# Performance work log

Measured on AMD Instinct MI355X. Metric: run time of the kernel, lower is better.

The kernel has to match this reference:

```python
import jax, jax.numpy as jnp
import numpy as np

SPATIAL_SHAPES = [(160, 160), (80, 80), (40, 40)]
D_MODEL = 256
N_HEADS = 8
N_LEVELS = 3
N_POINTS = 4
B = 1
SEQ = sum(h * w for h, w in SPATIAL_SHAPES)  # 33600


def setup_inputs() -> dict:
    key = jax.random.key(0)
    ks = jax.random.split(key, 10)
    f = jax.random.normal
    return {
        "hidden_states": f(ks[0], (B, SEQ, D_MODEL), jnp.float32),
        "encoder_hidden_states": f(ks[1], (B, SEQ, D_MODEL), jnp.float32),
        "position_embeddings": f(ks[2], (B, SEQ, D_MODEL), jnp.float32),
        "reference_points": jax.random.uniform(ks[3], (B, SEQ, N_LEVELS, 2), jnp.float32),
        "Wv": f(ks[4], (D_MODEL, D_MODEL), jnp.float32) * 0.02,
        "bv": jnp.zeros((D_MODEL,), jnp.float32),
        "Ws": f(ks[5], (N_HEADS * N_LEVELS * N_POINTS * 2, D_MODEL), jnp.float32) * 0.02,
        "bs": f(ks[6], (N_HEADS * N_LEVELS * N_POINTS * 2,), jnp.float32) * 2.0,
        "Wa": f(ks[7], (N_HEADS * N_LEVELS * N_POINTS, D_MODEL), jnp.float32) * 0.02,
        "ba": jnp.zeros((N_HEADS * N_LEVELS * N_POINTS,), jnp.float32),
        "Wo": f(ks[8], (D_MODEL, D_MODEL), jnp.float32) * 0.02,
        "bo": jnp.zeros((D_MODEL,), jnp.float32),
    }


def grid_sample_bilinear(img, grid):
    """torch.nn.functional.grid_sample, mode='bilinear', padding_mode='zeros', align_corners=False.
    img: [N, C, Hi, Wi]; grid: [N, Hg, Wg, 2] with (x, y) in [-1, 1]. Returns [N, C, Hg, Wg]."""
    N, C, Hi, Wi = img.shape
    x = (grid[..., 0] + 1.0) * (Wi * 0.5) - 0.5  # unnormalized pixel coords
    y = (grid[..., 1] + 1.0) * (Hi * 0.5) - 0.5
    x0f = jnp.floor(x)
    y0f = jnp.floor(y)
    x0 = x0f.astype(jnp.int32)
    y0 = y0f.astype(jnp.int32)
    wx1 = x - x0f
    wy1 = y - y0f
    imgc = jnp.transpose(img, (0, 2, 3, 1))  # [N, Hi, Wi, C]
    n_idx = jnp.arange(N)[:, None, None]

    def tap(xi, yi, w):
        valid = (xi >= 0) & (xi < Wi) & (yi >= 0) & (yi < Hi)
        xc = jnp.clip(xi, 0, Wi - 1)
        yc = jnp.clip(yi, 0, Hi - 1)
        v = imgc[n_idx, yc, xc]  # [N, Hg, Wg, C]
        return v * (w * valid.astype(img.dtype))[..., None]

    out = (tap(x0, y0, (1.0 - wx1) * (1.0 - wy1))
           + tap(x0 + 1, y0, wx1 * (1.0 - wy1))
           + tap(x0, y0 + 1, (1.0 - wx1) * wy1)
           + tap(x0 + 1, y0 + 1, wx1 * wy1))
    return jnp.transpose(out, (0, 3, 1, 2))  # [N, C, Hg, Wg]


def reference(hidden_states, encoder_hidden_states, position_embeddings, reference_points,
              Wv, bv, Ws, bs, Wa, ba, Wo, bo):
    hd = D_MODEL // N_HEADS
    LP = N_LEVELS * N_POINTS
    Q = SEQ

    hs = hidden_states + position_embeddings  # [B, Q, D]
    value = (encoder_hidden_states @ Wv.T + bv).reshape(B, SEQ, N_HEADS, hd)
    offsets = (hs @ Ws.T + bs).reshape(B * Q, N_HEADS, LP, 2)
    attn = jax.nn.softmax((hs @ Wa.T + ba).reshape(B, Q, N_HEADS, LP), axis=-1)

    # offset normalizer: [w, h] per level, broadcast over points
    norm = jnp.array([[w, h] for (h, w) in SPATIAL_SHAPES], jnp.float32)  # [L, 2]
    norm = jnp.broadcast_to(norm[:, None, :], (N_LEVELS, N_POINTS, 2)).reshape(1, 1, LP, 2)
    rp = reference_points.reshape(-1, N_LEVELS, 1, 2)
    rp = jnp.broadcast_to(rp, (B * Q, N_LEVELS, N_POINTS, 2)).reshape(B * Q, 1, LP, 2)
    loc = rp + offsets / norm                # [BQ, H, LP, 2]
    grids = 2.0 * loc - 1.0

    attn_t = jnp.transpose(attn, (0, 2, 1, 3)).reshape(B * N_HEADS, 1, Q, LP)

    sampled = []
    start = 0
    for lvl, (h, w) in enumerate(SPATIAL_SHAPES):
        v = value[:, start:start + h * w].reshape(B, h * w, N_HEADS * hd)
        v = jnp.transpose(v, (0, 2, 1)).reshape(B * N_HEADS, hd, h, w)
        g = jnp.transpose(grids[:, :, lvl * N_POINTS:(lvl + 1) * N_POINTS], (1, 0, 2, 3))  # [H, BQ, P, 2] (B=1)
        sampled.append(grid_sample_bilinear(v, g))  # [B*H, hd, Q, P]
        start += h * w

    out = (jnp.concatenate(sampled, axis=-1) * attn_t).sum(-1)  # [B*H, hd, Q]
    out = jnp.transpose(out.reshape(B, N_HEADS * hd, Q), (0, 2, 1))  # [B, Q, D]
    output = out @ Wo.T + bo
    return output, attn
```

## Files before the change

kernel.cpp:

```cpp
#include <hip/hip_runtime.h>
#include <math.h>

#define QSEQ 33600
#define NHEADS 8

typedef __attribute__((ext_vector_type(8))) short short8;
typedef __attribute__((ext_vector_type(4))) float floatx4;
typedef unsigned short ushort_t;

static __device__ __forceinline__ ushort_t f2bf(float f) {
  unsigned u = __float_as_uint(f);
  return (ushort_t)((u + 0x7FFF + ((u >> 16) & 1)) >> 16);
}

static __device__ __forceinline__ void gload_lds16(const void* g, void* l) {
  __builtin_amdgcn_global_load_lds((__attribute__((address_space(1))) void*)g,
                                   (__attribute__((address_space(3))) void*)l, 16, 0, 0);
}

template <int MODE>
__global__ __launch_bounds__(256) void gemm_mfma2(
    const ushort_t* __restrict__ A, const ushort_t* __restrict__ Wb,
    const float* __restrict__ bias, void* __restrict__ Cp, int N) {
  __shared__ ushort_t smem[12288];
  ushort_t* As = smem;
  ushort_t* Bs = smem + 4096;

  const int tid = threadIdx.x;
  const int m0 = blockIdx.y * 64;
  const int n0 = blockIdx.x * 128;
  const int wv = tid >> 6, lane = tid & 63;
  const int wm = wv >> 1, wn = wv & 1;
  const int l16 = lane & 15, quad = lane >> 4;

  const int ca0 = wv * 128 + lane, ca1 = ca0 + 64;
  const int ar0 = ca0 >> 3, ar1 = ca1 >> 3;
  const int ak0 = ((ca0 & 7) ^ (ar0 & 7)) * 8;
  const int ak1 = ((ca1 & 7) ^ (ar1 & 7)) * 8;
  const ushort_t* gA0 = A + (size_t)(m0 + ar0) * 256 + ak0;
  const ushort_t* gA1 = A + (size_t)(m0 + ar1) * 256 + ak1;
  ushort_t* lA0 = As + (wv * 128) * 8;
  ushort_t* lA1 = As + (wv * 128 + 64) * 8;

  const ushort_t* gB[4];
  ushort_t* lB[4];
#pragma unroll
  for (int j = 0; j < 4; ++j) {
    const int cb = wv * 256 + j * 64 + lane;
    const int br = cb >> 3;
    const int bk = ((cb & 7) ^ (br & 7)) * 8;
    gB[j] = Wb + (size_t)(n0 + br) * 256 + bk;
    lB[j] = Bs + (wv * 256 + j * 64) * 8;
  }

  floatx4 acc[2][4];
#pragma unroll
  for (int i = 0; i < 2; ++i)
#pragma unroll
    for (int j = 0; j < 4; ++j) acc[i][j] = (floatx4)(0.f);

  const int ra0 = wm * 32 + l16, ra1 = ra0 + 16;
  const int rb0 = wn * 64 + l16;
  const int l8 = l16 & 7;

  for (int k0 = 0; k0 < 256; k0 += 64) {
    gload_lds16(gA0 + k0, lA0);
    gload_lds16(gA1 + k0, lA1);
#pragma unroll
    for (int j = 0; j < 4; ++j) gload_lds16(gB[j] + k0, lB[j]);
    __syncthreads();
#pragma unroll
    for (int k32 = 0; k32 < 2; ++k32) {
      const int cx = ((k32 * 4 + quad) ^ l8) * 8;
      short8 a[2], b[4];
      a[0] = *(const short8*)&As[ra0 * 64 + cx];
      a[1] = *(const short8*)&As[ra1 * 64 + cx];
#pragma unroll
      for (int j = 0; j < 4; ++j)
        b[j] = *(const short8*)&Bs[(rb0 + j * 16) * 64 + cx];
#pragma unroll
      for (int mi = 0; mi < 2; ++mi)
#pragma unroll
        for (int ni = 0; ni < 4; ++ni)
          acc[mi][ni] = __builtin_amdgcn_mfma_f32_16x16x32_bf16(a[mi], b[ni], acc[mi][ni], 0, 0, 0);
    }
    __syncthreads();
  }

  if (MODE == 0) {
    float* C = (float*)Cp;
#pragma unroll
    for (int ni = 0; ni < 4; ++ni) {
      const int col = n0 + wn * 64 + ni * 16 + l16;
      if (col < N) {
        const float bia = bias[col];
#pragma unroll
        for (int mi = 0; mi < 2; ++mi) {
          const int rr = m0 + wm * 32 + mi * 16 + quad * 4;
#pragma unroll
          for (int r = 0; r < 4; ++r)
            C[(size_t)(rr + r) * N + col] = acc[mi][ni][r] + bia;
        }
      }
    }
  } else if (MODE == 1) {
    ushort_t* C = (ushort_t*)Cp;
#pragma unroll
    for (int ni = 0; ni < 4; ++ni) {
      const int col = n0 + wn * 64 + ni * 16 + l16;
      const float bia = bias[col];
      const int h = col >> 5, ch = col & 31;
#pragma unroll
      for (int mi = 0; mi < 2; ++mi) {
        const int rr = m0 + wm * 32 + mi * 16 + quad * 4;
#pragma unroll
        for (int r = 0; r < 4; ++r)
          C[((size_t)h * QSEQ + rr + r) * 32 + ch] = f2bf(acc[mi][ni][r] + bia);
      }
    }
  } else {
    float* smf = (float*)smem;
#pragma unroll
    for (int ni = 0; ni < 4; ++ni) {
      const int col = wn * 64 + ni * 16 + l16;
      if (col < 96) {
        const float bia = bias[col];
#pragma unroll
        for (int mi = 0; mi < 2; ++mi) {
          const int lr = wm * 32 + mi * 16 + quad * 4;
#pragma unroll
          for (int r = 0; r < 4; ++r)
            smf[(lr + r) * 96 + col] = acc[mi][ni][r] + bia;
        }
      }
    }
    __syncthreads();
    float* C = (float*)Cp;
#pragma unroll
    for (int p = 0; p < 2; ++p) {
      const int pair = tid * 2 + p;
      const int row = pair >> 3, hh = pair & 7;
      float v[12];
      float mx = -1e30f;
#pragma unroll
      for (int i = 0; i < 12; ++i) {
        v[i] = smf[row * 96 + hh * 12 + i];
        mx = fmaxf(mx, v[i]);
      }
      float s = 0.f;
#pragma unroll
      for (int i = 0; i < 12; ++i) {
        v[i] = __expf(v[i] - mx);
        s += v[i];
      }
      const float inv = 1.f / s;
      float4 o[3];
#pragma unroll
      for (int i = 0; i < 3; ++i) {
        o[i].x = v[i * 4 + 0] * inv;
        o[i].y = v[i * 4 + 1] * inv;
        o[i].z = v[i * 4 + 2] * inv;
        o[i].w = v[i * 4 + 3] * inv;
      }
      float4* dst = (float4*)&C[(size_t)(m0 + row) * 96 + hh * 12];
      dst[0] = o[0];
      dst[1] = o[1];
      dst[2] = o[2];
    }
  }
}

__global__ __launch_bounds__(256) void cvt_add_kernel(
    const float* __restrict__ a, const float* __restrict__ b, const float* __restrict__ e,
    ushort_t* __restrict__ hs, ushort_t* __restrict__ eb, int n8) {
  const int t = blockIdx.x * 256 + threadIdx.x;
  if (t >= n8) return;
  const float4* pa = (const float4*)(a + (size_t)t * 8);
  const float4* pb = (const float4*)(b + (size_t)t * 8);
  const float4* pe = (const float4*)(e + (size_t)t * 8);
  ushort_t t1[8], t2[8];
#pragma unroll
  for (int v = 0; v < 2; ++v) {
    const float4 x = pa[v], y = pb[v], z = pe[v];
    t1[v * 4 + 0] = f2bf(x.x + y.x);
    t1[v * 4 + 1] = f2bf(x.y + y.y);
    t1[v * 4 + 2] = f2bf(x.z + y.z);
    t1[v * 4 + 3] = f2bf(x.w + y.w);
    t2[v * 4 + 0] = f2bf(z.x);
    t2[v * 4 + 1] = f2bf(z.y);
    t2[v * 4 + 2] = f2bf(z.z);
    t2[v * 4 + 3] = f2bf(z.w);
  }
  *(uint4*)(hs + (size_t)t * 8) = *(const uint4*)t1;
  *(uint4*)(eb + (size_t)t * 8) = *(const uint4*)t2;
}

__global__ __launch_bounds__(256) void cvt_weights_kernel(
    const float* __restrict__ Wv, const float* __restrict__ Ws,
    const float* __restrict__ Wa, const float* __restrict__ Wo,
    ushort_t* __restrict__ o) {
  const int t = blockIdx.x * 256 + threadIdx.x;
  const int e = t * 4;
  if (e >= 204800) return;
  const float* src;
  int off;
  if (e < 65536)       { src = Wv; off = e; }
  else if (e < 114688) { src = Ws; off = e - 65536; }
  else if (e < 139264) { src = Wa; off = e - 114688; }
  else                 { src = Wo; off = e - 139264; }
  const float4 x = *(const float4*)(src + off);
  ushort_t tmp[4] = {f2bf(x.x), f2bf(x.y), f2bf(x.z), f2bf(x.w)};
  *(uint2*)(o + e) = *(const uint2*)tmp;
}

__global__ __launch_bounds__(256) void msda_sample_kernel(
    const ushort_t* __restrict__ value,
    const float* __restrict__ sp,
    const float* __restrict__ attn,
    const float* __restrict__ refp,
    ushort_t* __restrict__ outp) {
  const int h = blockIdx.x & 7;
  const int q = (blockIdx.x >> 3) * 4 + (threadIdx.x >> 6);
  const int lane = threadIdx.x & 63;
  const int cg = lane >> 4, pt = lane & 15;
  const int ptc = pt < 12 ? pt : 11;
  const int lvl = ptc >> 2;
  const int S = lvl == 0 ? 160 : (lvl == 1 ? 80 : 40);
  const int base = lvl == 0 ? 0 : (lvl == 1 ? 25600 : 32000);

  float a = attn[q * 96 + h * 12 + ptc];
  a = pt < 12 ? a : 0.f;
  const float2 off = *(const float2*)&sp[q * 192 + h * 24 + ptc * 2];
  const float2 rp = *(const float2*)&refp[q * 6 + lvl * 2];

  const float x = fmaf(rp.x, (float)S, off.x) - 0.5f;
  const float y = fmaf(rp.y, (float)S, off.y) - 0.5f;
  const float xf = floorf(x), yf = floorf(y);
  const int x0 = (int)xf, y0 = (int)yf;
  const float wx1 = x - xf, wy1 = y - yf;

  const float wx0z = (x0 >= 0 && x0 < S) ? 1.f - wx1 : 0.f;
  const float wx1z = (x0 + 1 >= 0 && x0 + 1 < S) ? wx1 : 0.f;
  const float wy0z = (y0 >= 0 && y0 < S) ? 1.f - wy1 : 0.f;
  const float wy1z = (y0 + 1 >= 0 && y0 + 1 < S) ? wy1 : 0.f;

  const int x0c = min(max(x0, 0), S - 1);
  const int x1c = min(max(x0 + 1, 0), S - 1);
  const int y0c = min(max(y0, 0), S - 1);
  const int y1c = min(max(y0 + 1, 0), S - 1);

  const float w00 = a * wx0z * wy0z, w10 = a * wx1z * wy0z;
  const float w01 = a * wx0z * wy1z, w11 = a * wx1z * wy1z;

  const ushort_t* hb = value + ((h * QSEQ + base) << 5) + cg * 8;
  const int r0 = y0c * S, r1 = y1c * S;
  const uint4 u00 = *(const uint4*)(hb + ((r0 + x0c) << 5));
  const uint4 u10 = *(const uint4*)(hb + ((r0 + x1c) << 5));
  const uint4 u01 = *(const uint4*)(hb + ((r1 + x0c) << 5));
  const uint4 u11 = *(const uint4*)(hb + ((r1 + x1c) << 5));

  float facc[8];
  {
    const unsigned a0[4] = {u00.x, u00.y, u00.z, u00.w};
    const unsigned a1[4] = {u10.x, u10.y, u10.z, u10.w};
    const unsigned a2[4] = {u01.x, u01.y, u01.z, u01.w};
    const unsigned a3[4] = {u11.x, u11.y, u11.z, u11.w};
#pragma unroll
    for (int i = 0; i < 4; ++i) {
      float lo = __uint_as_float(a0[i] << 16) * w00;
      float hi = __uint_as_float(a0[i] & 0xFFFF0000u) * w00;
      lo = fmaf(__uint_as_float(a1[i] << 16), w10, lo);
      hi = fmaf(__uint_as_float(a1[i] & 0xFFFF0000u), w10, hi);
      lo = fmaf(__uint_as_float(a2[i] << 16), w01, lo);
      hi = fmaf(__uint_as_float(a2[i] & 0xFFFF0000u), w01, hi);
      lo = fmaf(__uint_as_float(a3[i] << 16), w11, lo);
      hi = fmaf(__uint_as_float(a3[i] & 0xFFFF0000u), w11, hi);
      facc[2 * i + 0] = lo;
      facc[2 * i + 1] = hi;
    }
  }

#pragma unroll
  for (int m = 1; m < 16; m <<= 1)
#pragma unroll
    for (int i = 0; i < 8; ++i) facc[i] += __shfl_xor(facc[i], m, 64);

  if (pt == 0) {
    ushort_t t[8];
#pragma unroll
    for (int i = 0; i < 8; ++i) t[i] = f2bf(facc[i]);
    *(uint4*)&outp[(size_t)q * 256 + h * 32 + cg * 8] = *(const uint4*)t;
  }
}

extern "C" void kernel_launch(void* const* d_in, const int* in_sizes, int n_in,
                              void* d_out, int out_size, void* d_ws, size_t ws_size,
                              hipStream_t stream) {
  const float* hidden = (const float*)d_in[0];
  const float* ehs    = (const float*)d_in[1];
  const float* pos    = (const float*)d_in[2];
  const float* refp   = (const float*)d_in[3];
  const float* Wv = (const float*)d_in[4];
  const float* bv = (const float*)d_in[5];
  const float* Ws = (const float*)d_in[6];
  const float* bs = (const float*)d_in[7];
  const float* Wa = (const float*)d_in[8];
  const float* ba = (const float*)d_in[9];
  const float* Wo = (const float*)d_in[10];
  const float* bo = (const float*)d_in[11];

  float* out  = (float*)d_out;
  float* attn = out + (size_t)QSEQ * 256;

  char* ws = (char*)d_ws;
  ushort_t* ws_value = (ushort_t*)ws;
  ushort_t* ws_hs    = ws_value + (size_t)QSEQ * 256;
  ushort_t* ws_outp  = ws_hs + (size_t)QSEQ * 256;
  ushort_t* ws_w     = ws_outp + (size_t)QSEQ * 256;
  float* ws_sp = (float*)(ws_w + 204800);

  ushort_t* Wv_b = ws_w;
  ushort_t* Ws_b = ws_w + 65536;
  ushort_t* Wa_b = ws_w + 114688;
  ushort_t* Wo_b = ws_w + 139264;

  dim3 blk(256);

  cvt_weights_kernel<<<dim3(200), blk, 0, stream>>>(Wv, Ws, Wa, Wo, ws_w);
  cvt_add_kernel<<<dim3(4200), blk, 0, stream>>>(hidden, pos, ehs, ws_hs, ws_outp, QSEQ * 256 / 8);

  gemm_mfma2<1><<<dim3(2, 525), blk, 0, stream>>>(ws_outp, Wv_b, bv, ws_value, 256);
  gemm_mfma2<0><<<dim3(2, 525), blk, 0, stream>>>(ws_hs, Ws_b, bs, ws_sp, 192);
  gemm_mfma2<2><<<dim3(1, 525), blk, 0, stream>>>(ws_hs, Wa_b, ba, attn, 96);
  msda_sample_kernel<<<dim3((QSEQ / 4) * 8), blk, 0, stream>>>(ws_value, ws_sp, attn, refp, ws_outp);
  gemm_mfma2<0><<<dim3(2, 525), blk, 0, stream>>>(ws_outp, Wo_b, bo, out, 256);
}
```

Baseline: 327.0 us.

## Fuse fp32→bf16 conversion into GEMM loads and merge offset/attention GEMMs

```diff
diff --git a/kernel.cpp b/kernel.cpp
--- a/kernel.cpp
+++ b/kernel.cpp
@@ -18,68 +18,98 @@
                                    (__attribute__((address_space(3))) void*)l, 16, 0, 0);
 }
 
-template <int MODE>
-__global__ __launch_bounds__(256) void gemm_mfma2(
-    const ushort_t* __restrict__ A, const ushort_t* __restrict__ Wb,
-    const float* __restrict__ bias, void* __restrict__ Cp, int N) {
-  __shared__ ushort_t smem[12288];
+template <int ASRC, int MODE>
+__global__ __launch_bounds__(256) void gemm96(
+    const void* __restrict__ A1, const float* __restrict__ A2,
+    const ushort_t* __restrict__ Wb, const float* __restrict__ b1,
+    const float* __restrict__ b2, void* __restrict__ C1,
+    float* __restrict__ C2, int N) {
+  extern __shared__ ushort_t smem[];
   ushort_t* As = smem;
-  ushort_t* Bs = smem + 4096;
+  ushort_t* Bs = smem + 6144;
 
   const int tid = threadIdx.x;
-  const int m0 = blockIdx.y * 64;
+  const int m0 = blockIdx.y * 96;
   const int n0 = blockIdx.x * 128;
   const int wv = tid >> 6, lane = tid & 63;
   const int wm = wv >> 1, wn = wv & 1;
   const int l16 = lane & 15, quad = lane >> 4;
-
-  const int ca0 = wv * 128 + lane, ca1 = ca0 + 64;
-  const int ar0 = ca0 >> 3, ar1 = ca1 >> 3;
-  const int ak0 = ((ca0 & 7) ^ (ar0 & 7)) * 8;
-  const int ak1 = ((ca1 & 7) ^ (ar1 & 7)) * 8;
-  const ushort_t* gA0 = A + (size_t)(m0 + ar0) * 256 + ak0;
-  const ushort_t* gA1 = A + (size_t)(m0 + ar1) * 256 + ak1;
-  ushort_t* lA0 = As + (wv * 128) * 8;
-  ushort_t* lA1 = As + (wv * 128 + 64) * 8;
-
+  const int l8 = l16 & 7;
+
+  const ushort_t* gAb[3];
+  ushort_t* lAb[3];
+  const float* gAf[3];
+  const float* gAf2[3];
+  ushort_t* lAf[3];
+#pragma unroll
+  for (int i = 0; i < 3; ++i) {
+    const int c = tid + i * 256;
+    const int row = c >> 3, s = c & 7;
+    if (ASRC == 0) {
+      const int gch = s ^ (row & 7);
+      gAb[i] = (const ushort_t*)A1 + (size_t)(m0 + row) * 256 + gch * 8;
+      lAb[i] = As + (wv * 64 + i * 256) * 8;
+    } else {
+      gAf[i] = (const float*)A1 + (size_t)(m0 + row) * 256 + s * 8;
+      if (ASRC == 2) gAf2[i] = A2 + (size_t)(m0 + row) * 256 + s * 8;
+      lAf[i] = As + row * 64 + (s ^ (row & 7)) * 8;
+    }
+  }
   const ushort_t* gB[4];
   ushort_t* lB[4];
 #pragma unroll
   for (int j = 0; j < 4; ++j) {
     const int cb = wv * 256 + j * 64 + lane;
     const int br = cb >> 3;
-    const int bk = ((cb & 7) ^ (br & 7)) * 8;
-    gB[j] = Wb + (size_t)(n0 + br) * 256 + bk;
+    const int gch = (cb & 7) ^ (br & 7);
+    gB[j] = Wb + (size_t)(n0 + br) * 256 + gch * 8;
     lB[j] = Bs + (wv * 256 + j * 64) * 8;
   }
 
-  floatx4 acc[2][4];
-#pragma unroll
-  for (int i = 0; i < 2; ++i)
+  floatx4 acc[3][4];
+#pragma unroll
+  for (int i = 0; i < 3; ++i)
 #pragma unroll
     for (int j = 0; j < 4; ++j) acc[i][j] = (floatx4)(0.f);
 
-  const int ra0 = wm * 32 + l16, ra1 = ra0 + 16;
-  const int rb0 = wn * 64 + l16;
-  const int l8 = l16 & 7;
-
   for (int k0 = 0; k0 < 256; k0 += 64) {
-    gload_lds16(gA0 + k0, lA0);
-    gload_lds16(gA1 + k0, lA1);
+    if (ASRC == 0) {
+#pragma unroll
+      for (int i = 0; i < 3; ++i) gload_lds16(gAb[i] + k0, lAb[i]);
+    } else {
+#pragma unroll
+      for (int i = 0; i < 3; ++i) {
+        const float4 x0 = *(const float4*)(gAf[i] + k0);
+        const float4 x1 = *(const float4*)(gAf[i] + k0 + 4);
+        float v[8] = {x0.x, x0.y, x0.z, x0.w, x1.x, x1.y, x1.z, x1.w};
+        if (ASRC == 2) {
+          const float4 y0 = *(const float4*)(gAf2[i] + k0);
+          const float4 y1 = *(const float4*)(gAf2[i] + k0 + 4);
+          v[0] += y0.x; v[1] += y0.y; v[2] += y0.z; v[3] += y0.w;
+          v[4] += y1.x; v[5] += y1.y; v[6] += y1.z; v[7] += y1.w;
+        }
+        ushort_t t[8];
+#pragma unroll
+        for (int e = 0; e < 8; ++e) t[e] = f2bf(v[e]);
+        *(short8*)lAf[i] = *(const short8*)t;
+      }
+    }
 #pragma unroll
     for (int j = 0; j < 4; ++j) gload_lds16(gB[j] + k0, lB[j]);
     __syncthreads();
+
 #pragma unroll
     for (int k32 = 0; k32 < 2; ++k32) {
       const int cx = ((k32 * 4 + quad) ^ l8) * 8;
-      short8 a[2], b[4];
-      a[0] = *(const short8*)&As[ra0 * 64 + cx];
-      a[1] = *(const short8*)&As[ra1 * 64 + cx];
-#pragma unroll
-      for (int j = 0; j < 4; ++j)
-        b[j] = *(const short8*)&Bs[(rb0 + j * 16) * 64 + cx];
-#pragma unroll
-      for (int mi = 0; mi < 2; ++mi)
+      short8 a[3], b[4];
+#pragma unroll
+      for (int mi = 0; mi < 3; ++mi)
+        a[mi] = *(const short8*)&As[(wm * 48 + mi * 16 + l16) * 64 + cx];
+#pragma unroll
+      for (int ni = 0; ni < 4; ++ni)
+        b[ni] = *(const short8*)&Bs[(wn * 64 + ni * 16 + l16) * 64 + cx];
+#pragma unroll
+      for (int mi = 0; mi < 3; ++mi)
 #pragma unroll
         for (int ni = 0; ni < 4; ++ni)
           acc[mi][ni] = __builtin_amdgcn_mfma_f32_16x16x32_bf16(a[mi], b[ni], acc[mi][ni], 0, 0, 0);
@@ -88,31 +118,29 @@
   }
 
   if (MODE == 0) {
-    float* C = (float*)Cp;
+    float* C = (float*)C1;
 #pragma unroll
     for (int ni = 0; ni < 4; ++ni) {
       const int col = n0 + wn * 64 + ni * 16 + l16;
-      if (col < N) {
-        const float bia = bias[col];
-#pragma unroll
-        for (int mi = 0; mi < 2; ++mi) {
-          const int rr = m0 + wm * 32 + mi * 16 + quad * 4;
-#pragma unroll
-          for (int r = 0; r < 4; ++r)
-            C[(size_t)(rr + r) * N + col] = acc[mi][ni][r] + bia;
-        }
+      const float bia = b1[col];
+#pragma unroll
+      for (int mi = 0; mi < 3; ++mi) {
+        const int rr = m0 + wm * 48 + mi * 16 + quad * 4;
+#pragma unroll
+        for (int r = 0; r < 4; ++r)
+          C[(size_t)(rr + r) * N + col] = acc[mi][ni][r] + bia;
       }
     }
   } else if (MODE == 1) {
-    ushort_t* C = (ushort_t*)Cp;
+    ushort_t* C = (ushort_t*)C1;
 #pragma unroll
     for (int ni = 0; ni < 4; ++ni) {
       const int col = n0 + wn * 64 + ni * 16 + l16;
-      const float bia = bias[col];
+      const float bia = b1[col];
       const int h = col >> 5, ch = col & 31;
 #pragma unroll
-      for (int mi = 0; mi < 2; ++mi) {
-        const int rr = m0 + wm * 32 + mi * 16 + quad * 4;
+      for (int mi = 0; mi < 3; ++mi) {
+        const int rr = m0 + wm * 48 + mi * 16 + quad * 4;
 #pragma unroll
         for (int r = 0; r < 4; ++r)
           C[((size_t)h * QSEQ + rr + r) * 32 + ch] = f2bf(acc[mi][ni][r] + bia);
@@ -122,77 +150,63 @@
     float* smf = (float*)smem;
 #pragma unroll
     for (int ni = 0; ni < 4; ++ni) {
-      const int col = wn * 64 + ni * 16 + l16;
+      const int col = n0 + wn * 64 + ni * 16 + l16;
       if (col < 96) {
-        const float bia = bias[col];
-#pragma unroll
-        for (int mi = 0; mi < 2; ++mi) {
-          const int lr = wm * 32 + mi * 16 + quad * 4;
+        const float bia = b1[col];
+#pragma unroll
+        for (int mi = 0; mi < 3; ++mi) {
+          const int lr = wm * 48 + mi * 16 + quad * 4;
 #pragma unroll
           for (int r = 0; r < 4; ++r)
             smf[(lr + r) * 96 + col] = acc[mi][ni][r] + bia;
         }
+      } else if (col < 288) {
+        const float bia = b2[col - 96];
+#pragma unroll
+        for (int mi = 0; mi < 3; ++mi) {
+          const int rr = m0 + wm * 48 + mi * 16 + quad * 4;
+#pragma unroll
+          for (int r = 0; r < 4; ++r)
+            C2[(size_t)(rr + r) * 192 + (col - 96)] = acc[mi][ni][r] + bia;
+        }
       }
     }
     __syncthreads();
-    float* C = (float*)Cp;
-#pragma unroll
-    for (int p = 0; p < 2; ++p) {
-      const int pair = tid * 2 + p;
-      const int row = pair >> 3, hh = pair & 7;
-      float v[12];
-      float mx = -1e30f;
-#pragma unroll
-      for (int i = 0; i < 12; ++i) {
-        v[i] = smf[row * 96 + hh * 12 + i];
-        mx = fmaxf(mx, v[i]);
-      }
-      float s = 0.f;
-#pragma unroll
-      for (int i = 0; i < 12; ++i) {
-        v[i] = __expf(v[i] - mx);
-        s += v[i];
-      }
-      const float inv = 1.f / s;
-      float4 o[3];
-#pragma unroll
-      for (int i = 0; i < 3; ++i) {
-        o[i].x = v[i * 4 + 0] * inv;
-        o[i].y = v[i * 4 + 1] * inv;
-        o[i].z = v[i * 4 + 2] * inv;
-        o[i].w = v[i * 4 + 3] * inv;
-      }
-      float4* dst = (float4*)&C[(size_t)(m0 + row) * 96 + hh * 12];
-      dst[0] = o[0];
-      dst[1] = o[1];
-      dst[2] = o[2];
-    }
-  }
-}
-
-__global__ __launch_bounds__(256) void cvt_add_kernel(
-    const float* __restrict__ a, const float* __restrict__ b, const float* __restrict__ e,
-    ushort_t* __restrict__ hs, ushort_t* __restrict__ eb, int n8) {
-  const int t = blockIdx.x * 256 + threadIdx.x;
-  if (t >= n8) return;
-  const float4* pa = (const float4*)(a + (size_t)t * 8);
-  const float4* pb = (const float4*)(b + (size_t)t * 8);
-  const float4* pe = (const float4*)(e + (size_t)t * 8);
-  ushort_t t1[8], t2[8];
-#pragma unroll
-  for (int v = 0; v < 2; ++v) {
-    const float4 x = pa[v], y = pb[v], z = pe[v];
-    t1[v * 4 + 0] = f2bf(x.x + y.x);
-    t1[v * 4 + 1] = f2bf(x.y + y.y);
-    t1[v * 4 + 2] = f2bf(x.z + y.z);
-    t1[v * 4 + 3] = f2bf(x.w + y.w);
-    t2[v * 4 + 0] = f2bf(z.x);
-    t2[v * 4 + 1] = f2bf(z.y);
-    t2[v * 4 + 2] = f2bf(z.z);
-    t2[v * 4 + 3] = f2bf(z.w);
-  }
-  *(uint4*)(hs + (size_t)t * 8) = *(const uint4*)t1;
-  *(uint4*)(eb + (size_t)t * 8) = *(const uint4*)t2;
+    if (blockIdx.x == 0) {
+      float* C = (float*)C1;
+#pragma unroll
+      for (int p = 0; p < 3; ++p) {
+        const int task = tid + p * 256;
+        const int row = task >> 3, hh = task & 7;
+        float v[12];
+        float mx = -1e30f;
+#pragma unroll
+        for (int i = 0; i < 12; ++i) {
+          v[i] = smf[row * 96 + hh * 12 + i];
+          mx = fmaxf(mx, v[i]);
+        }
+        float s = 0.f;
+#pragma unroll
+        for (int i = 0; i < 12; ++i) {
+          v[i] = __expf(v[i] - mx);
+          s += v[i];
+        }
+        const float inv = 1.f / s;
+        float4 o[3];
+#pragma unroll
+        for (int i = 0; i < 3; ++i) {
+          o[i].x = v[i * 4 + 0] * inv;
+          o[i].y = v[i * 4 + 1] * inv;
+          o[i].z = v[i * 4 + 2] * inv;
+          o[i].w = v[i * 4 + 3] * inv;
+        }
+        float4* dst = (float4*)&C[(size_t)(m0 + row) * 96 + hh * 12];
+        dst[0] = o[0];
+        dst[1] = o[1];
+        dst[2] = o[2];
+      }
+    }
+  }
 }
 
 __global__ __launch_bounds__(256) void cvt_weights_kernel(
@@ -205,8 +219,8 @@
   const float* src;
   int off;
   if (e < 65536)       { src = Wv; off = e; }
-  else if (e < 114688) { src = Ws; off = e - 65536; }
-  else if (e < 139264) { src = Wa; off = e - 114688; }
+  else if (e < 90112)  { src = Wa; off = e - 65536; }
+  else if (e < 139264) { src = Ws; off = e - 90112; }
   else                 { src = Wo; off = e - 139264; }
   const float4 x = *(const float4*)(src + off);
   ushort_t tmp[4] = {f2bf(x.x), f2bf(x.y), f2bf(x.z), f2bf(x.w)};
@@ -314,24 +328,20 @@
 
   char* ws = (char*)d_ws;
   ushort_t* ws_value = (ushort_t*)ws;
-  ushort_t* ws_hs    = ws_value + (size_t)QSEQ * 256;
-  ushort_t* ws_outp  = ws_hs + (size_t)QSEQ * 256;
+  ushort_t* ws_outp  = ws_value + (size_t)QSEQ * 256;
   ushort_t* ws_w     = ws_outp + (size_t)QSEQ * 256;
   float* ws_sp = (float*)(ws_w + 204800);
 
   ushort_t* Wv_b = ws_w;
-  ushort_t* Ws_b = ws_w + 65536;
-  ushort_t* Wa_b = ws_w + 114688;
+  ushort_t* Wm_b = ws_w + 65536;
   ushort_t* Wo_b = ws_w + 139264;
 
   dim3 blk(256);
 
   cvt_weights_kernel<<<dim3(200), blk, 0, stream>>>(Wv, Ws, Wa, Wo, ws_w);
-  cvt_add_kernel<<<dim3(4200), blk, 0, stream>>>(hidden, pos, ehs, ws_hs, ws_outp, QSEQ * 256 / 8);
-
-  gemm_mfma2<1><<<dim3(2, 525), blk, 0, stream>>>(ws_outp, Wv_b, bv, ws_value, 256);
-  gemm_mfma2<0><<<dim3(2, 525), blk, 0, stream>>>(ws_hs, Ws_b, bs, ws_sp, 192);
-  gemm_mfma2<2><<<dim3(1, 525), blk, 0, stream>>>(ws_hs, Wa_b, ba, attn, 96);
+
+  gemm96<1, 1><<<dim3(2, 350), blk, 28672, stream>>>(ehs, nullptr, Wv_b, bv, nullptr, ws_value, nullptr, 256);
+  gemm96<2, 2><<<dim3(3, 350), blk, 36864, stream>>>(hidden, pos, Wm_b, ba, bs, attn, ws_sp, 288);
   msda_sample_kernel<<<dim3((QSEQ / 4) * 8), blk, 0, stream>>>(ws_value, ws_sp, attn, refp, ws_outp);
-  gemm_mfma2<0><<<dim3(2, 525), blk, 0, stream>>>(ws_outp, Wo_b, bo, out, 256);
-}
+  gemm96<0, 0><<<dim3(2, 350), blk, 28672, stream>>>(ws_outp, nullptr, Wo_b, bo, nullptr, out, nullptr, 256);
+}
```

After: 312.0 us. 4.6% less time.
